# Performance work log

Measured on AMD Instinct MI355X. Metric: run time of the kernel, lower is better.

The kernel has to match this reference:

```python
import jax, jax.numpy as jnp
import numpy as np

EMB_DIM = 1024
ATT_DIM = 1024
N_HEADS = 16
HEAD_DIM = ATT_DIM // N_HEADS
ROPE_THETA = 10000.0


def setup_inputs() -> dict:
    key = jax.random.key(0)
    k1, k2, k3 = jax.random.split(key, 3)
    B, S = 2, 2048
    x = jax.random.normal(k1, (B, S, EMB_DIM), dtype=jnp.float32)
    # nn.Linear weights stored as [in, out] for x @ W
    W_qkv = jax.random.normal(k2, (EMB_DIM, 3 * ATT_DIM), dtype=jnp.float32) / np.sqrt(EMB_DIM)
    W_out = jax.random.normal(k3, (ATT_DIM, EMB_DIM), dtype=jnp.float32) / np.sqrt(ATT_DIM)
    return {"x": x, "W_qkv": W_qkv, "W_out": W_out}


def _rope_cos_sin(seq_len, dim, dtype):
    # rotary-embedding-torch: freqs over even indices, repeated interleaved
    inv_freq = 1.0 / (ROPE_THETA ** (jnp.arange(0, dim, 2, dtype=jnp.float32) / dim))
    t = jnp.arange(seq_len, dtype=jnp.float32)
    freqs = t[:, None] * inv_freq[None, :]            # [S, dim/2]
    freqs = jnp.repeat(freqs, 2, axis=-1)             # [S, dim] interleaved
    return jnp.cos(freqs).astype(dtype), jnp.sin(freqs).astype(dtype)


def _rotate_half(x):
    # interleaved pairs: (x0, x1) -> (-x1, x0)
    xr = x.reshape(x.shape[:-1] + (x.shape[-1] // 2, 2))
    x1, x2 = xr[..., 0], xr[..., 1]
    return jnp.stack([-x2, x1], axis=-1).reshape(x.shape)


def _apply_rope(x, cos, sin):
    # x: [B, H, S, D]; cos/sin: [S, D]
    return x * cos[None, None] + _rotate_half(x) * sin[None, None]


def reference(x, W_qkv, W_out):
    B, S, _ = x.shape
    qkv = x @ W_qkv                                   # [B, S, 3*ATT]
    qkv = qkv.reshape(B, S, 3, N_HEADS, HEAD_DIM)
    qkv = jnp.moveaxis(qkv, 3, 1)                     # [B, H, S, 3, D]
    q, k, v = qkv[..., 0, :], qkv[..., 1, :], qkv[..., 2, :]

    cos, sin = _rope_cos_sin(S, HEAD_DIM, x.dtype)
    q = _apply_rope(q, cos, sin)
    k = _apply_rope(k, cos, sin)

    scale = 1.0 / np.sqrt(HEAD_DIM)
    scores = jnp.einsum("bhqd,bhkd->bhqk", q, k) * scale
    attn = jax.nn.softmax(scores, axis=-1)
    out = jnp.einsum("bhqk,bhkd->bhqd", attn, v)      # [B, H, S, D]
    out = jnp.moveaxis(out, 1, 2).reshape(B, S, ATT_DIM)
    return out @ W_out                                # [B, S, EMB_DIM]
```

## Files before the change

### kernel.cpp

```cpp
#include <hip/hip_runtime.h>
#include <cstdint>
#include <cstddef>

typedef unsigned short u16;
typedef __bf16 bf16x8 __attribute__((ext_vector_type(8)));
typedef float f32x4 __attribute__((ext_vector_type(4)));
typedef unsigned int u32x4 __attribute__((ext_vector_type(4)));

#define DEVI __device__ __forceinline__

constexpr int SEQ = 2048, NH = 16, HD = 64, EMB = 1024, N3 = 3072, MROWS = 4096;

DEVI u16 f2bf(float f) {
    union { float f; unsigned u; } x; x.f = f;
    unsigned r = (x.u + 0x7fffu + ((x.u >> 16) & 1u)) >> 16;
    return (u16)r;
}

DEVI f32x4 mfma16(bf16x8 a, bf16x8 b, f32x4 c) {
    return __builtin_amdgcn_mfma_f32_16x16x32_bf16(a, b, c, 0, 0, 0);
}

DEVI float exp2_raw(float x) {
    float r;
    asm("v_exp_f32 %0, %1" : "=v"(r) : "v"(x));
    return r;
}

#define GLDS16(g, l)                                                          \
    __builtin_amdgcn_global_load_lds(                                         \
        (__attribute__((address_space(1))) void*)(g),                         \
        (__attribute__((address_space(3))) void*)(l), 16, 0, 0)

__global__ __launch_bounds__(256) void prep_k(const float* __restrict__ x,
                                              const float* __restrict__ wqk,
                                              const float* __restrict__ wo,
                                              u16* __restrict__ xb, u16* __restrict__ wqkvT,
                                              u16* __restrict__ woutT, float2* __restrict__ tab) {
    __shared__ float tile[64][65];
    int bid = blockIdx.x, tid = threadIdx.x;
    if (bid < 4096) {
        int i = bid * 256 + tid;
        float4 v = ((const float4*)x)[i];
        ushort4 o;
        o.x = f2bf(v.x); o.y = f2bf(v.y); o.z = f2bf(v.z); o.w = f2bf(v.w);
        ((ushort4*)xb)[i] = o;
    } else if (bid < 5120) {
        const float* in; u16* out; int N, bx, by;
        if (bid < 4864) { in = wqk; out = wqkvT; N = 3072; int bb = bid - 4096; bx = bb % 48; by = bb / 48; }
        else            { in = wo;  out = woutT; N = 1024; int bb = bid - 4864; bx = bb % 16; by = bb / 16; }
        const int K = 1024;
        int k0 = by * 64, n0 = bx * 64;
        for (int i = 0; i < 16; i++) {
            int idx = i * 256 + tid;
            int r = idx >> 6, c = idx & 63;
            tile[r][c] = in[(size_t)(k0 + r) * N + n0 + c];
        }
        __syncthreads();
        for (int i = 0; i < 16; i++) {
            int idx = i * 256 + tid;
            int n = idx >> 6, k = idx & 63;
            out[(size_t)(n0 + n) * K + k0 + k] = f2bf(tile[k][n]);
        }
    } else {
        int idx = (bid - 5120) * 256 + tid;
        int t = idx >> 5, i = idx & 31;
        double ang = (double)t * pow(10000.0, -(double)i / 32.0);
        tab[idx] = make_float2((float)cos(ang), (float)sin(ang));
    }
}

template <int EPI>
__global__ __launch_bounds__(256, 4) void gemm128_k(const u16* __restrict__ A, const u16* __restrict__ Bt,
                                                    int Kd, int Ncols,
                                                    u16* __restrict__ q_out, u16* __restrict__ k_out,
                                                    u16* __restrict__ v_out,
                                                    const float2* __restrict__ tab,
                                                    float* __restrict__ Cout) {
    __shared__ __align__(16) u16 smem[17408];
    u16* As0 = smem;
    u16* As1 = smem + 4096;
    u16* Bs0 = smem + 8192;
    u16* Bs1 = smem + 12288;
    int tid = threadIdx.x, lane = tid & 63, wv = tid >> 6;
    int wr = wv >> 1, wc = wv & 1;
    int l15 = lane & 15, lg = lane >> 4;
    int fr = (l15 >> 1) & 3;

    int nwg = gridDim.x * gridDim.y;
    int bid = blockIdx.y * gridDim.x + blockIdx.x;
    int swzb = (bid & 7) * (nwg >> 3) + (bid >> 3);
    int bx = swzb % gridDim.x, by = swzb / gridDim.x;
    int brow = by * 128, bcol = bx * 128;

    f32x4 acc[4][4];
    for (int i = 0; i < 4; i++)
        for (int j = 0; j < 4; j++) acc[i][j] = (f32x4){0.f, 0.f, 0.f, 0.f};

    const u16* aptr[2];
    const u16* bptr[2];
#pragma unroll
    for (int i = 0; i < 2; i++) {
        int cidx = i * 256 + tid;
        int rrow = cidx >> 2, cc = cidx & 3;
        int sw = (cc ^ ((rrow >> 1) & 3)) * 8;
        aptr[i] = A + (size_t)(brow + rrow) * Kd + sw;
        bptr[i] = Bt + (size_t)(bcol + rrow) * Kd + sw;
    }

    auto stageG = [&](u16* Ad, u16* Bd) {
#pragma unroll
        for (int i = 0; i < 2; i++) {
            GLDS16(aptr[i], Ad + (i * 256 + tid) * 8);
            GLDS16(bptr[i], Bd + (i * 256 + tid) * 8);
            aptr[i] += 32;
            bptr[i] += 32;
        }
    };

    auto computeT = [&](const u16* Ar, const u16* Br) {
        bf16x8 af[4], bf[4];
#pragma unroll
        for (int mi = 0; mi < 4; mi++)
            af[mi] = *(const bf16x8*)&Ar[(wr * 64 + mi * 16 + l15) * 32 + (lg ^ fr) * 8];
#pragma unroll
        for (int ni = 0; ni < 4; ni++)
            bf[ni] = *(const bf16x8*)&Br[(wc * 64 + ni * 16 + l15) * 32 + (lg ^ fr) * 8];
#pragma unroll
        for (int mi = 0; mi < 4; mi++)
#pragma unroll
            for (int ni = 0; ni < 4; ni++)
                acc[mi][ni] = mfma16(af[mi], bf[ni], acc[mi][ni]);
    };

    int nIter = Kd >> 5;
    stageG(As0, Bs0);
    for (int it = 0; it < nIter; it += 2) {
        __syncthreads();
        if (it + 1 < nIter) stageG(As1, Bs1);
        computeT(As0, Bs0);
        __syncthreads();
        if (it + 2 < nIter) stageG(As0, Bs0);
        computeT(As1, Bs1);
    }

    if constexpr (EPI == 0) {
        int c = bcol >> 10;
        int bb = brow >> 11, sbase = brow & 2047;
        int hbase = (bcol & 1023) >> 6;
        if (c == 2) {
            for (int mi = 0; mi < 4; mi++)
                for (int ni = 0; ni < 4; ni++) {
                    int col = wc * 64 + ni * 16 + l15;
                    int d = col & 63, h2 = col >> 6;
                    int s0 = sbase + wr * 64 + mi * 16 + lg * 4;
                    ushort4 pw;
                    pw.x = f2bf(acc[mi][ni][0]);
                    pw.y = f2bf(acc[mi][ni][1]);
                    pw.z = f2bf(acc[mi][ni][2]);
                    pw.w = f2bf(acc[mi][ni][3]);
                    *(ushort4*)&v_out[((size_t)(bb * NH + hbase + h2) * HD + d) * SEQ + s0] = pw;
                }
        } else {
            u16* dst = (c == 0) ? q_out : k_out;
            float sc = (c == 0) ? 0.125f * 1.4426950408889634f : 1.0f;
            u16* ep = smem;
            __syncthreads();
            for (int mi = 0; mi < 4; mi++)
                for (int ni = 0; ni < 4; ni++) {
                    int col = wc * 64 + ni * 16 + l15;
                    int dg = col & 63;
                    for (int r = 0; r < 4; r++) {
                        int rowl = wr * 64 + mi * 16 + lg * 4 + r;
                        int s = sbase + rowl;
                        float val = acc[mi][ni][r];
                        float part = __shfl_xor(val, 1);
                        float2 cs = tab[(s << 5) | (dg >> 1)];
                        float o = (dg & 1) ? (val * cs.x + part * cs.y)
                                           : (val * cs.x - part * cs.y);
                        ep[rowl * 136 + (col ^ ((rowl & 7) << 3))] = f2bf(o * sc);
                    }
                }
            __syncthreads();
#pragma unroll
            for (int p = 0; p < 8; p++) {
                int unit = p * 32 + (tid >> 3);
                int h2 = unit >> 7, s_r = unit & 127, j = tid & 7;
                int cj = (h2 * 8 + j) ^ (s_r & 7);
                uint4 w = *(const uint4*)&ep[s_r * 136 + cj * 8];
                *(uint4*)&dst[(((size_t)(bb * NH + hbase + h2) * SEQ + sbase + s_r) << 6) +
                              j * 8] = w;
            }
        }
    } else {
        for (int mi = 0; mi < 4; mi++)
            for (int ni = 0; ni < 4; ni++) {
                int col = bcol + wc * 64 + ni * 16 + l15;
                for (int r = 0; r < 4; r++) {
                    int row = brow + wr * 64 + mi * 16 + lg * 4 + r;
                    Cout[(size_t)row * Ncols + col] = acc[mi][ni][r];
                }
            }
    }
}

__global__ __launch_bounds__(256, 2) void attn8_k(const u16* __restrict__ Qb,
                                                  const u16* __restrict__ Kb,
                                                  const u16* __restrict__ Vtg,
                                                  u16* __restrict__ Ob) {
    __shared__ __align__(16) u16 Ks[2][64 * 64];
    __shared__ __align__(16) u16 Vs[2][64 * 64];
    int tid = threadIdx.x, lane = tid & 63, wv = tid >> 6;
    int l15 = lane & 15, lg = lane >> 4;
    int fk = (l15 & 3) | (((l15 >> 2) & 1) << 2);
    int fv = (l15 & 3) | (((l15 >> 3) & 1) << 2);
    int bh = blockIdx.y, b = bh >> 4, h = bh & 15;
    int qbase = blockIdx.x * 128;
    const size_t base = (size_t)bh * SEQ * HD;

    int c0 = tid, c1 = 256 + tid;
    int r0 = c0 >> 3, s0 = ((c0 & 7) ^ ((r0 & 3) | ((r0 >> 1) & 4))) * 8;
    int r1 = c1 >> 3, s1 = ((c1 & 7) ^ ((r1 & 3) | ((r1 >> 1) & 4))) * 8;
    const u16* kp0 = Kb + base + r0 * HD + s0;
    const u16* kp1 = Kb + base + r1 * HD + s1;
    const u16* vp0 = Vtg + base + (size_t)r0 * SEQ + s0;
    const u16* vp1 = Vtg + base + (size_t)r1 * SEQ + s1;

    bf16x8 qf[2][2];
#pragma unroll
    for (int u = 0; u < 2; u++)
#pragma unroll
        for (int kt = 0; kt < 2; kt++)
            qf[u][kt] = *(const bf16x8*)&Qb[base + (size_t)(qbase + wv * 32 + u * 16 + l15) * HD +
                                            kt * 32 + lg * 8];

    f32x4 oacc[2][4];
    float Lp[2] = {0.f, 0.f};
#pragma unroll
    for (int u = 0; u < 2; u++)
#pragma unroll
        for (int nt = 0; nt < 4; nt++) oacc[u][nt] = (f32x4){0.f, 0.f, 0.f, 0.f};

    auto stage = [&](int buf) {
        GLDS16(kp0, &Ks[buf][c0 * 8]);
        GLDS16(kp1, &Ks[buf][c1 * 8]);
        GLDS16(vp0, &Vs[buf][c0 * 8]);
        GLDS16(vp1, &Vs[buf][c1 * 8]);
        kp0 += 64 * HD; kp1 += 64 * HD;
        vp0 += 64; vp1 += 64;
    };

    stage(0);

    for (int it = 0; it < 32; ++it) {
        int buf = it & 1;
        __syncthreads();
        if (it < 31) stage(buf ^ 1);

        bf16x8 kf[4][2], vf[4][2];
#pragma unroll
        for (int nt = 0; nt < 4; nt++) {
            int rk = ((nt >> 1) << 5) + ((l15 >> 2) << 3) + ((nt & 1) << 2) + (l15 & 3);
#pragma unroll
            for (int kt = 0; kt < 2; kt++) {
                kf[nt][kt] = *(const bf16x8*)&Ks[buf][rk * 64 + (((kt * 4 + lg) ^ fk)) * 8];
                vf[nt][kt] = *(const bf16x8*)&Vs[buf][(nt * 16 + l15) * 64 +
                                                     (((kt * 4 + lg) ^ fv)) * 8];
            }
        }

        unsigned pk[2][4][2];
#pragma unroll
        for (int u = 0; u < 2; u++) {
            f32x4 sa[4];
            __builtin_amdgcn_s_setprio(1);
#pragma unroll
            for (int nt = 0; nt < 4; nt++) {
                f32x4 z = (f32x4){0.f, 0.f, 0.f, 0.f};
#pragma unroll
                for (int kt = 0; kt < 2; kt++) z = mfma16(kf[nt][kt], qf[u][kt], z);
                sa[nt] = z;
            }
            __builtin_amdgcn_s_setprio(0);
            float ls = 0.f;
#pragma unroll
            for (int nt = 0; nt < 4; nt++) {
                float e0 = exp2_raw(sa[nt][0]), e1 = exp2_raw(sa[nt][1]);
                float e2 = exp2_raw(sa[nt][2]), e3 = exp2_raw(sa[nt][3]);
                ls += (e0 + e1) + (e2 + e3);
                asm("v_cvt_pk_bf16_f32 %0, %1, %2" : "=v"(pk[u][nt][0]) : "v"(e0), "v"(e1));
                asm("v_cvt_pk_bf16_f32 %0, %1, %2" : "=v"(pk[u][nt][1]) : "v"(e2), "v"(e3));
            }
            Lp[u] += ls;
        }

        bf16x8 pa[2][2];
#pragma unroll
        for (int u = 0; u < 2; u++)
#pragma unroll
            for (int kt = 0; kt < 2; kt++) {
                u32x4 t = {pk[u][2 * kt][0], pk[u][2 * kt][1], pk[u][2 * kt + 1][0],
                           pk[u][2 * kt + 1][1]};
                pa[u][kt] = __builtin_bit_cast(bf16x8, t);
            }
        __builtin_amdgcn_s_setprio(1);
#pragma unroll
        for (int kt = 0; kt < 2; kt++)
#pragma unroll
            for (int nt = 0; nt < 4; nt++)
#pragma unroll
                for (int u = 0; u < 2; u++)
                    oacc[u][nt] = mfma16(pa[u][kt], vf[nt][kt], oacc[u][nt]);
        __builtin_amdgcn_s_setprio(0);
    }

    float linv[2][4];
#pragma unroll
    for (int u = 0; u < 2; u++) {
        float L = Lp[u];
        L += __shfl_xor(L, 16);
        L += __shfl_xor(L, 32);
#pragma unroll
        for (int r = 0; r < 4; r++) linv[u][r] = 1.0f / __shfl(L, lg * 4 + r);
    }
#pragma unroll
    for (int u = 0; u < 2; u++)
#pragma unroll
        for (int nt = 0; nt < 4; nt++)
#pragma unroll
            for (int r = 0; r < 4; r++) {
                int row = qbase + wv * 32 + u * 16 + lg * 4 + r;
                Ob[(size_t)(b * SEQ + row) * EMB + h * HD + nt * 16 + l15] =
                    f2bf(oacc[u][nt][r] * linv[u][r]);
            }
}


extern "C" void kernel_launch(void* const* d_in, const int* in_sizes, int n_in,
                              void* d_out, int out_size, void* d_ws, size_t ws_size,
                              hipStream_t stream) {
    const float* x = (const float*)d_in[0];
    const float* wqk = (const float*)d_in[1];
    const float* wo = (const float*)d_in[2];
    float* out = (float*)d_out;
    char* ws = (char*)d_ws;

    u16* xb = (u16*)(ws + 0);
    u16* wqkvT = (u16*)(ws + 8388608);
    u16* woutT = (u16*)(ws + 14680064);
    u16* qb = (u16*)(ws + 16777216);
    u16* kb = (u16*)(ws + 25165824);
    u16* vb = (u16*)(ws + 33554432);
    u16* ao = (u16*)(ws + 41943040);
    float2* tab = (float2*)(ws + 50331648);

    prep_k<<<5376, 256, 0, stream>>>(x, wqk, wo, xb, wqkvT, woutT, tab);
    gemm128_k<0><<<dim3(N3 / 128, MROWS / 128), 256, 0, stream>>>(xb, wqkvT, EMB, N3, qb, kb, vb,
                                                                  tab, nullptr);
    attn8_k<<<dim3(SEQ / 128, 2 * NH), 256, 0, stream>>>(qb, kb, vb, ao);
    gemm128_k<1><<<dim3(EMB / 128, MROWS / 128), 256, 0, stream>>>(ao, woutT, EMB, EMB, nullptr,
                                                                   nullptr, nullptr, nullptr, out);
}
```

Baseline: 108.8 us.

## Use triple-buffered LDS pipeline with partial vmcnt waits in GEMM and attention

Replaces the double-buffered global-to-LDS staging in both the GEMM and attention kernels with a three-stage ring buffer. Each step waits only for the older load group via s_waitcnt vmcnt(4) and a raw barrier, so two tiles can be in flight while one is computed. This hides more memory latency, but LDS per block goes up, and the GEMM occupancy hint drops from 4 to 3 blocks per CU. The loop is unrolled for exactly 32 K-iterations, which holds for both GEMM calls (K=1024) and for attention (2048/64).

New measurement: 104.6 us (median of 2 runs). -3.8%, faster.

```diff
diff --git a/kernel.cpp b/kernel.cpp
--- a/kernel.cpp
+++ b/kernel.cpp
@@ -31,6 +31,15 @@
     __builtin_amdgcn_global_load_lds(                                         \
         (__attribute__((address_space(1))) void*)(g),                         \
         (__attribute__((address_space(3))) void*)(l), 16, 0, 0)
+
+#define GWAIT4 asm volatile("s_waitcnt vmcnt(4)" ::: "memory")
+#define GWAIT0 asm volatile("s_waitcnt vmcnt(0)" ::: "memory")
+#define RBAR                                                                  \
+    do {                                                                      \
+        __builtin_amdgcn_sched_barrier(0);                                    \
+        __builtin_amdgcn_s_barrier();                                         \
+        __builtin_amdgcn_sched_barrier(0);                                    \
+    } while (0)
 
 __global__ __launch_bounds__(256) void prep_k(const float* __restrict__ x,
                                               const float* __restrict__ wqk,
@@ -71,17 +80,13 @@
 }
 
 template <int EPI>
-__global__ __launch_bounds__(256, 4) void gemm128_k(const u16* __restrict__ A, const u16* __restrict__ Bt,
+__global__ __launch_bounds__(256, 3) void gemm128_k(const u16* __restrict__ A, const u16* __restrict__ Bt,
                                                     int Kd, int Ncols,
                                                     u16* __restrict__ q_out, u16* __restrict__ k_out,
                                                     u16* __restrict__ v_out,
                                                     const float2* __restrict__ tab,
                                                     float* __restrict__ Cout) {
-    __shared__ __align__(16) u16 smem[17408];
-    u16* As0 = smem;
-    u16* As1 = smem + 4096;
-    u16* Bs0 = smem + 8192;
-    u16* Bs1 = smem + 12288;
+    __shared__ __align__(16) u16 smem[24576];
     int tid = threadIdx.x, lane = tid & 63, wv = tid >> 6;
     int wr = wv >> 1, wc = wv & 1;
     int l15 = lane & 15, lg = lane >> 4;
@@ -108,17 +113,19 @@
         bptr[i] = Bt + (size_t)(bcol + rrow) * Kd + sw;
     }
 
-    auto stageG = [&](u16* Ad, u16* Bd) {
+    auto stageG = [&](u16* base) {
 #pragma unroll
         for (int i = 0; i < 2; i++) {
-            GLDS16(aptr[i], Ad + (i * 256 + tid) * 8);
-            GLDS16(bptr[i], Bd + (i * 256 + tid) * 8);
+            GLDS16(aptr[i], base + (i * 256 + tid) * 8);
+            GLDS16(bptr[i], base + 4096 + (i * 256 + tid) * 8);
             aptr[i] += 32;
             bptr[i] += 32;
         }
     };
 
-    auto computeT = [&](const u16* Ar, const u16* Br) {
+    auto computeT = [&](const u16* base) {
+        const u16* Ar = base;
+        const u16* Br = base + 4096;
         bf16x8 af[4], bf[4];
 #pragma unroll
         for (int mi = 0; mi < 4; mi++)
@@ -133,16 +140,19 @@
                 acc[mi][ni] = mfma16(af[mi], bf[ni], acc[mi][ni]);
     };
 
-    int nIter = Kd >> 5;
-    stageG(As0, Bs0);
-    for (int it = 0; it < nIter; it += 2) {
-        __syncthreads();
-        if (it + 1 < nIter) stageG(As1, Bs1);
-        computeT(As0, Bs0);
-        __syncthreads();
-        if (it + 2 < nIter) stageG(As0, Bs0);
-        computeT(As1, Bs1);
-    }
+    u16* b0 = smem;
+    u16* b1 = smem + 8192;
+    u16* b2 = smem + 16384;
+
+    stageG(b0);
+    stageG(b1);
+    for (int r = 0; r < 10; ++r) {
+        GWAIT4; RBAR; stageG(b2); computeT(b0);
+        GWAIT4; RBAR; stageG(b0); computeT(b1);
+        GWAIT4; RBAR; stageG(b1); computeT(b2);
+    }
+    GWAIT4; RBAR; computeT(b0);
+    GWAIT0; RBAR; computeT(b1);
 
     if constexpr (EPI == 0) {
         int c = bcol >> 10;
@@ -204,12 +214,12 @@
     }
 }
 
-__global__ __launch_bounds__(256, 2) void attn8_k(const u16* __restrict__ Qb,
+__global__ __launch_bounds__(256, 2) void attn9_k(const u16* __restrict__ Qb,
                                                   const u16* __restrict__ Kb,
                                                   const u16* __restrict__ Vtg,
                                                   u16* __restrict__ Ob) {
-    __shared__ __align__(16) u16 Ks[2][64 * 64];
-    __shared__ __align__(16) u16 Vs[2][64 * 64];
+    __shared__ __align__(16) u16 Ks[3][64 * 64];
+    __shared__ __align__(16) u16 Vs[3][64 * 64];
     int tid = threadIdx.x, lane = tid & 63, wv = tid >> 6;
     int l15 = lane & 15, lg = lane >> 4;
     int fk = (l15 & 3) | (((l15 >> 2) & 1) << 2);
@@ -241,31 +251,25 @@
 #pragma unroll
         for (int nt = 0; nt < 4; nt++) oacc[u][nt] = (f32x4){0.f, 0.f, 0.f, 0.f};
 
-    auto stage = [&](int buf) {
-        GLDS16(kp0, &Ks[buf][c0 * 8]);
-        GLDS16(kp1, &Ks[buf][c1 * 8]);
-        GLDS16(vp0, &Vs[buf][c0 * 8]);
-        GLDS16(vp1, &Vs[buf][c1 * 8]);
+    auto stage = [&](u16* Kd, u16* Vd) {
+        GLDS16(kp0, Kd + c0 * 8);
+        GLDS16(kp1, Kd + c1 * 8);
+        GLDS16(vp0, Vd + c0 * 8);
+        GLDS16(vp1, Vd + c1 * 8);
         kp0 += 64 * HD; kp1 += 64 * HD;
         vp0 += 64; vp1 += 64;
     };
 
-    stage(0);
-
-    for (int it = 0; it < 32; ++it) {
-        int buf = it & 1;
-        __syncthreads();
-        if (it < 31) stage(buf ^ 1);
-
+    auto body = [&](const u16* Kl, const u16* Vl) {
         bf16x8 kf[4][2], vf[4][2];
 #pragma unroll
         for (int nt = 0; nt < 4; nt++) {
             int rk = ((nt >> 1) << 5) + ((l15 >> 2) << 3) + ((nt & 1) << 2) + (l15 & 3);
 #pragma unroll
             for (int kt = 0; kt < 2; kt++) {
-                kf[nt][kt] = *(const bf16x8*)&Ks[buf][rk * 64 + (((kt * 4 + lg) ^ fk)) * 8];
-                vf[nt][kt] = *(const bf16x8*)&Vs[buf][(nt * 16 + l15) * 64 +
-                                                     (((kt * 4 + lg) ^ fv)) * 8];
+                kf[nt][kt] = *(const bf16x8*)&Kl[rk * 64 + (((kt * 4 + lg) ^ fk)) * 8];
+                vf[nt][kt] = *(const bf16x8*)&Vl[(nt * 16 + l15) * 64 +
+                                                (((kt * 4 + lg) ^ fv)) * 8];
             }
         }
 
@@ -312,7 +316,17 @@
                 for (int u = 0; u < 2; u++)
                     oacc[u][nt] = mfma16(pa[u][kt], vf[nt][kt], oacc[u][nt]);
         __builtin_amdgcn_s_setprio(0);
-    }
+    };
+
+    stage(Ks[0], Vs[0]);
+    stage(Ks[1], Vs[1]);
+    for (int r = 0; r < 10; ++r) {
+        GWAIT4; RBAR; stage(Ks[2], Vs[2]); body(Ks[0], Vs[0]);
+        GWAIT4; RBAR; stage(Ks[0], Vs[0]); body(Ks[1], Vs[1]);
+        GWAIT4; RBAR; stage(Ks[1], Vs[1]); body(Ks[2], Vs[2]);
+    }
+    GWAIT4; RBAR; body(Ks[0], Vs[0]);
+    GWAIT0; RBAR; body(Ks[1], Vs[1]);
 
     float linv[2][4];
 #pragma unroll
@@ -357,7 +371,7 @@
     prep_k<<<5376, 256, 0, stream>>>(x, wqk, wo, xb, wqkvT, woutT, tab);
     gemm128_k<0><<<dim3(N3 / 128, MROWS / 128), 256, 0, stream>>>(xb, wqkvT, EMB, N3, qb, kb, vb,
                                                                   tab, nullptr);
-    attn8_k<<<dim3(SEQ / 128, 2 * NH), 256, 0, stream>>>(qb, kb, vb, ao);
+    attn9_k<<<dim3(SEQ / 128, 2 * NH), 256, 0, stream>>>(qb, kb, vb, ao);
     gemm128_k<1><<<dim3(EMB / 128, MROWS / 128), 256, 0, stream>>>(ao, woutT, EMB, EMB, nullptr,
                                                                    nullptr, nullptr, nullptr, out);
 }
```
